# Kernel tuning notes

Hardware: AMD Instinct MI355X
Metric: run time of the kernel (lower is better)

The kernel has to match this reference:

```python
import jax, jax.numpy as jnp
import numpy as np

# config (matches cfg init_kwargs)
FG_THRESH = 0.5
BG_THRESH_LO = 0.1
BG_THRESH_HI = 0.5
N_FG_ROIS = 128
N_ROIS = 512
MEAN = np.array([0.0, 0.0, 0.0, 0.0], dtype=np.float32)
STD = np.array([0.2, 0.2, 0.2, 0.2], dtype=np.float32)

N_PROP = 262144
N_GT = 128


def _make_boxes(key, n, img=1024.0):
    k1, k2 = jax.random.split(key)
    xy = jax.random.uniform(k1, (n, 2), dtype=jnp.float32) * (img - 64.0)
    wh = jax.random.uniform(k2, (n, 2), dtype=jnp.float32) * 192.0 + 8.0
    return jnp.concatenate([xy, xy + wh], axis=-1)  # [n,4] valid x1y1x2y2


def setup_inputs() -> dict:
    key = jax.random.key(0)
    k1, k2, k3 = jax.random.split(key, 3)
    rois = _make_boxes(k1, N_PROP)[None]          # [1, N, 4]
    gt_bbox = _make_boxes(k2, N_GT)[None]         # [1, G, 4]
    labels = jax.random.randint(k3, (1, N_GT), 0, 81, dtype=jnp.int32)  # [1, G]
    return {"rois": rois, "gt_bbox": gt_bbox, "labels": labels}


def _iou_matrix(boxes, gt):
    # boxes [M,4], gt [G,4] -> [M,G] IoU with +1 pixel convention
    bx1, by1, bx2, by2 = boxes[:, 0:1], boxes[:, 1:2], boxes[:, 2:3], boxes[:, 3:4]
    gx1, gy1, gx2, gy2 = gt[None, :, 0], gt[None, :, 1], gt[None, :, 2], gt[None, :, 3]
    iw = jnp.clip(jnp.minimum(bx2, gx2) - jnp.maximum(bx1, gx1) + 1.0, 0.0)
    ih = jnp.clip(jnp.minimum(by2, gy2) - jnp.maximum(by1, gy1) + 1.0, 0.0)
    inter = iw * ih
    area_b = (bx2 - bx1 + 1.0) * (by2 - by1 + 1.0)          # [M,1]
    area_g = (gx2 - gx1 + 1.0) * (gy2 - gy1 + 1.0)          # [1,G]
    return inter / (area_b + area_g - inter)


def _bbox_transform(rois, gt):
    w = rois[:, 2] - rois[:, 0] + 1.0
    h = rois[:, 3] - rois[:, 1] + 1.0
    cx = rois[:, 0] + 0.5 * w
    cy = rois[:, 1] + 0.5 * h
    gw = gt[:, 2] - gt[:, 0] + 1.0
    gh = gt[:, 3] - gt[:, 1] + 1.0
    gcx = gt[:, 0] + 0.5 * gw
    gcy = gt[:, 1] + 0.5 * gh
    return jnp.stack([(gcx - cx) / w, (gcy - cy) / h,
                      jnp.log(gw / w), jnp.log(gh / h)], axis=1)


def _forward(rois, gt_bbox, labels):
    rois = rois[0]          # [N,4]
    gt = gt_bbox[0]         # [G,4]
    lab = labels[0]         # [G]
    all_rois = jnp.concatenate([rois, gt], axis=0)          # [M,4], M=N+G
    ious = _iou_matrix(all_rois, gt)                        # [M,G]  <- dominant traffic
    argmax_row = jnp.argmax(ious, axis=1)                   # [M]
    max_row = jnp.max(ious, axis=1)                         # [M]

    fg = max_row > FG_THRESH
    bg = (max_row > BG_THRESH_LO) & (max_row < BG_THRESH_HI)

    # fixed-size, deterministic variant of the fg/bg sampling:
    # keep first min(N_FG_ROIS, #fg) fg, then fill with bg up to N_ROIS
    fg_cum = jnp.cumsum(fg.astype(jnp.int32))
    sel_fg = fg & (fg_cum <= N_FG_ROIS)
    n_fg = jnp.minimum(N_FG_ROIS, fg_cum[-1])
    bg_cum = jnp.cumsum(bg.astype(jnp.int32))
    sel_bg = bg & (bg_cum <= (N_ROIS - n_fg))

    # stable sort key: fg first (0), then bg (1), then padding rows (2)
    key = jnp.where(sel_fg, 0, jnp.where(sel_bg, 1, 2)).astype(jnp.int32)
    order = jnp.argsort(key, stable=True)
    idx = order[:N_ROIS]                                    # [N_ROIS]

    rois_out = jnp.take(all_rois, idx, axis=0)              # [N_ROIS,4]
    gt_idx = jnp.take(argmax_row, idx)
    labels_out = jnp.take(lab, gt_idx)                      # [N_ROIS]
    gt_out = jnp.take(gt, gt_idx, axis=0)

    delta = _bbox_transform(rois_out, gt_out)
    delta = (delta - jnp.asarray(MEAN)) / jnp.asarray(STD)  # intended normalization
    return rois_out, delta, labels_out


def reference(rois, gt_bbox, labels):
    return _forward(rois, gt_bbox, labels)
```

## Files before the change

### kernel.cpp

```cpp
#include <hip/hip_runtime.h>
#include <stdint.h>

#define N_PROP    262144
#define N_GT      128
#define N_ALL     (N_PROP + N_GT)
#define NFG_MAX   128
#define NROIS_OUT 512
#define BLK       256
#define NBLOCKS   ((N_ALL + BLK - 1) / BLK)

#define OFF_ARGMAX  0
#define OFF_FLAG    524544
#define OFF_BLOCKFG 786816
#define OFF_BLOCKBG 790916
#define OFF_FGOFF   795016
#define OFF_BGOFF   799116
#define OFF_PARAMS  803216

__global__ __launch_bounds__(BLK) void k_iou(
    const float* __restrict__ rois, const float* __restrict__ gt,
    uint16_t* __restrict__ argmax, uint8_t* __restrict__ flag,
    int* __restrict__ blockFg, int* __restrict__ blockBg)
{
    __shared__ float sgx1[N_GT], sgy1[N_GT], sgx2[N_GT], sgy2[N_GT], sga[N_GT];
    int tid = threadIdx.x;
    for (int j = tid; j < N_GT; j += BLK) {
        float4 g = *reinterpret_cast<const float4*>(gt + 4 * j);
        sgx1[j] = g.x; sgy1[j] = g.y; sgx2[j] = g.z; sgy2[j] = g.w;
        sga[j] = __fmul_rn(__fadd_rn(__fsub_rn(g.z, g.x), 1.0f),
                           __fadd_rn(__fsub_rn(g.w, g.y), 1.0f));
    }
    __syncthreads();

    int i = blockIdx.x * BLK + tid;
    bool valid = (i < N_ALL);
    float bx1 = 0.f, by1 = 0.f, bx2 = 0.f, by2 = 0.f;
    if (valid) {
        const float* p = (i < N_PROP) ? (rois + 4 * (size_t)i)
                                      : (gt + 4 * (size_t)(i - N_PROP));
        float4 b = *reinterpret_cast<const float4*>(p);
        bx1 = b.x; by1 = b.y; bx2 = b.z; by2 = b.w;
    }
    float area_b = __fmul_rn(__fadd_rn(__fsub_rn(bx2, bx1), 1.0f),
                             __fadd_rn(__fsub_rn(by2, by1), 1.0f));
    float best = -1.0f; int bestj = 0;
    if (valid) {
        #pragma unroll 4
        for (int j = 0; j < N_GT; ++j) {
            float iw = fmaxf(__fadd_rn(__fsub_rn(fminf(bx2, sgx2[j]), fmaxf(bx1, sgx1[j])), 1.0f), 0.0f);
            float ih = fmaxf(__fadd_rn(__fsub_rn(fminf(by2, sgy2[j]), fmaxf(by1, sgy1[j])), 1.0f), 0.0f);
            float inter = __fmul_rn(iw, ih);
            float denom = __fsub_rn(__fadd_rn(area_b, sga[j]), inter);
            float iou = __fdiv_rn(inter, denom);
            if (iou > best) { best = iou; bestj = j; }
        }
    }
    bool fg = valid && (best > 0.5f);
    bool bg = valid && (best > 0.1f) && (best < 0.5f);
    if (valid) {
        argmax[i] = (uint16_t)bestj;
        flag[i]   = fg ? (uint8_t)0 : (bg ? (uint8_t)1 : (uint8_t)2);
    }
    unsigned long long mf = __ballot(fg ? 1 : 0);
    unsigned long long mb = __ballot(bg ? 1 : 0);
    __shared__ int sF[BLK / 64], sB[BLK / 64];
    int lane = tid & 63, w = tid >> 6;
    if (lane == 0) { sF[w] = __popcll(mf); sB[w] = __popcll(mb); }
    __syncthreads();
    if (tid == 0) {
        int tf = 0, tb = 0;
        for (int k = 0; k < BLK / 64; ++k) { tf += sF[k]; tb += sB[k]; }
        blockFg[blockIdx.x] = tf;
        blockBg[blockIdx.x] = tb;
    }
}

__global__ __launch_bounds__(BLK) void k_scan(
    const int* __restrict__ blockFg, const int* __restrict__ blockBg,
    int* __restrict__ fgOff, int* __restrict__ bgOff, int* __restrict__ params)
{
    __shared__ int sF[BLK], sB[BLK];
    int tid = threadIdx.x;
    int carryF = 0, carryB = 0;
    for (int base = 0; base < NBLOCKS; base += BLK) {
        int idx = base + tid;
        int f = (idx < NBLOCKS) ? blockFg[idx] : 0;
        int b = (idx < NBLOCKS) ? blockBg[idx] : 0;
        sF[tid] = f; sB[tid] = b;
        __syncthreads();
        for (int off = 1; off < BLK; off <<= 1) {
            int vf = (tid >= off) ? sF[tid - off] : 0;
            int vb = (tid >= off) ? sB[tid - off] : 0;
            __syncthreads();
            sF[tid] += vf; sB[tid] += vb;
            __syncthreads();
        }
        if (idx < NBLOCKS) {
            fgOff[idx] = carryF + sF[tid] - f;
            bgOff[idx] = carryB + sB[tid] - b;
        }
        carryF += sF[BLK - 1];
        carryB += sB[BLK - 1];
        __syncthreads();
    }
    if (tid == 0) {
        int fgTot = carryF, bgTot = carryB;
        int NF  = fgTot < NFG_MAX ? fgTot : NFG_MAX;
        int LIM = NROIS_OUT - NF;
        int NB  = bgTot < LIM ? bgTot : LIM;
        params[0] = NF; params[1] = NB; params[2] = LIM;
    }
}

__global__ __launch_bounds__(BLK) void k_select(
    const float* __restrict__ rois, const float* __restrict__ gt,
    const int* __restrict__ labels,
    const uint16_t* __restrict__ argmax, const uint8_t* __restrict__ flag,
    const int* __restrict__ fgOff, const int* __restrict__ bgOff,
    const int* __restrict__ params, float* __restrict__ out)
{
    int tid = threadIdx.x;
    int i = blockIdx.x * BLK + tid;
    bool valid = (i < N_ALL);
    uint8_t f = valid ? flag[i] : (uint8_t)2;
    bool isfg = valid && (f == 0);
    bool isbg = valid && (f == 1);
    unsigned long long mf = __ballot(isfg ? 1 : 0);
    unsigned long long mb = __ballot(isbg ? 1 : 0);
    int lane = tid & 63, w = tid >> 6;
    unsigned long long lemask = (lane == 63) ? ~0ull : ((1ull << (lane + 1)) - 1ull);
    int inclF = __popcll(mf & lemask);
    int inclB = __popcll(mb & lemask);
    __shared__ int sF[BLK / 64], sB[BLK / 64];
    if (lane == 0) { sF[w] = __popcll(mf); sB[w] = __popcll(mb); }
    __syncthreads();
    int preF = 0, preB = 0;
    for (int k = 0; k < w; ++k) { preF += sF[k]; preB += sB[k]; }
    if (!valid) return;

    int fgCum = fgOff[blockIdx.x] + preF + inclF;
    int bgCum = bgOff[blockIdx.x] + preB + inclB;
    int NF = params[0], NB = params[1], LIM = params[2];

    int pos;
    if (isfg && fgCum <= NFG_MAX) {
        pos = fgCum - 1;
    } else if (isbg && bgCum <= LIM) {
        pos = NF + bgCum - 1;
    } else {
        int selF = fgCum < NFG_MAX ? fgCum : NFG_MAX;
        int selB = bgCum < LIM ? bgCum : LIM;
        int restCum = (i + 1) - selF - selB;
        pos = NF + NB + restCum - 1;
    }
    if (pos >= NROIS_OUT) return;

    const float* rp = (i < N_PROP) ? (rois + 4 * (size_t)i)
                                   : (gt + 4 * (size_t)(i - N_PROP));
    float4 r = *reinterpret_cast<const float4*>(rp);
    int g = argmax[i];
    float4 gb = *reinterpret_cast<const float4*>(gt + 4 * (size_t)g);

    float wdt = __fadd_rn(__fsub_rn(r.z, r.x), 1.0f);
    float hgt = __fadd_rn(__fsub_rn(r.w, r.y), 1.0f);
    float cx  = __fadd_rn(r.x, __fmul_rn(0.5f, wdt));
    float cy  = __fadd_rn(r.y, __fmul_rn(0.5f, hgt));
    float gw  = __fadd_rn(__fsub_rn(gb.z, gb.x), 1.0f);
    float gh  = __fadd_rn(__fsub_rn(gb.w, gb.y), 1.0f);
    float gcx = __fadd_rn(gb.x, __fmul_rn(0.5f, gw));
    float gcy = __fadd_rn(gb.y, __fmul_rn(0.5f, gh));

    float d0 = __fdiv_rn(__fsub_rn(gcx, cx), wdt);
    float d1 = __fdiv_rn(__fsub_rn(gcy, cy), hgt);
    float d2 = logf(__fdiv_rn(gw, wdt));
    float d3 = logf(__fdiv_rn(gh, hgt));
    d0 = __fdiv_rn(d0, 0.2f);
    d1 = __fdiv_rn(d1, 0.2f);
    d2 = __fdiv_rn(d2, 0.2f);
    d3 = __fdiv_rn(d3, 0.2f);

    out[4 * pos + 0] = r.x;
    out[4 * pos + 1] = r.y;
    out[4 * pos + 2] = r.z;
    out[4 * pos + 3] = r.w;
    out[2048 + 4 * pos + 0] = d0;
    out[2048 + 4 * pos + 1] = d1;
    out[2048 + 4 * pos + 2] = d2;
    out[2048 + 4 * pos + 3] = d3;
    out[4096 + pos] = (float)labels[g];
}

extern "C" void kernel_launch(void* const* d_in, const int* in_sizes, int n_in,
                              void* d_out, int out_size, void* d_ws, size_t ws_size,
                              hipStream_t stream)
{
    const float* rois   = (const float*)d_in[0];
    const float* gt     = (const float*)d_in[1];
    const int*   labels = (const int*)d_in[2];
    float* out = (float*)d_out;

    char* ws = (char*)d_ws;
    uint16_t* argmax  = (uint16_t*)(ws + OFF_ARGMAX);
    uint8_t*  flag    = (uint8_t*)(ws + OFF_FLAG);
    int*      blockFg = (int*)(ws + OFF_BLOCKFG);
    int*      blockBg = (int*)(ws + OFF_BLOCKBG);
    int*      fgOff   = (int*)(ws + OFF_FGOFF);
    int*      bgOff   = (int*)(ws + OFF_BGOFF);
    int*      params  = (int*)(ws + OFF_PARAMS);

    k_iou<<<NBLOCKS, BLK, 0, stream>>>(rois, gt, argmax, flag, blockFg, blockBg);
    k_scan<<<1, BLK, 0, stream>>>(blockFg, blockBg, fgOff, bgOff, params);
    k_select<<<NBLOCKS, BLK, 0, stream>>>(rois, gt, labels, argmax, flag,
                                          fgOff, bgOff, params, out);
}
```

Measured before the change: 46.56 us.

## Drop scan kernel; compute block prefix offsets redundantly in select kernel

Removes the single-block scan kernel. Each select block now reduces all packed per-block fg/bg counts itself to get its prefix and the totals. It also packs argmax and flag into one 16-bit word, which cuts a global read and write. This saves one launch and a serial single-block stage, at the cost of every one of the ~1025 blocks reading the whole 4 KB count array.

```diff
diff --git a/kernel.cpp b/kernel.cpp
--- a/kernel.cpp
+++ b/kernel.cpp
@@ -9,18 +9,12 @@
 #define BLK       256
 #define NBLOCKS   ((N_ALL + BLK - 1) / BLK)
 
-#define OFF_ARGMAX  0
-#define OFF_FLAG    524544
-#define OFF_BLOCKFG 786816
-#define OFF_BLOCKBG 790916
-#define OFF_FGOFF   795016
-#define OFF_BGOFF   799116
-#define OFF_PARAMS  803216
+#define OFF_PACKED 0
+#define OFF_CNT    524544
 
 __global__ __launch_bounds__(BLK) void k_iou(
     const float* __restrict__ rois, const float* __restrict__ gt,
-    uint16_t* __restrict__ argmax, uint8_t* __restrict__ flag,
-    int* __restrict__ blockFg, int* __restrict__ blockBg)
+    uint16_t* __restrict__ packed, uint32_t* __restrict__ cnt)
 {
     __shared__ float sgx1[N_GT], sgy1[N_GT], sgx2[N_GT], sgy2[N_GT], sga[N_GT];
     int tid = threadIdx.x;
@@ -58,8 +52,8 @@
     bool fg = valid && (best > 0.5f);
     bool bg = valid && (best > 0.1f) && (best < 0.5f);
     if (valid) {
-        argmax[i] = (uint16_t)bestj;
-        flag[i]   = fg ? (uint8_t)0 : (bg ? (uint8_t)1 : (uint8_t)2);
+        int flagv = fg ? 0 : (bg ? 1 : 2);
+        packed[i] = (uint16_t)((flagv << 8) | bestj);
     }
     unsigned long long mf = __ballot(fg ? 1 : 0);
     unsigned long long mb = __ballot(bg ? 1 : 0);
@@ -70,77 +64,68 @@
     if (tid == 0) {
         int tf = 0, tb = 0;
         for (int k = 0; k < BLK / 64; ++k) { tf += sF[k]; tb += sB[k]; }
-        blockFg[blockIdx.x] = tf;
-        blockBg[blockIdx.x] = tb;
-    }
-}
-
-__global__ __launch_bounds__(BLK) void k_scan(
-    const int* __restrict__ blockFg, const int* __restrict__ blockBg,
-    int* __restrict__ fgOff, int* __restrict__ bgOff, int* __restrict__ params)
-{
-    __shared__ int sF[BLK], sB[BLK];
-    int tid = threadIdx.x;
-    int carryF = 0, carryB = 0;
-    for (int base = 0; base < NBLOCKS; base += BLK) {
-        int idx = base + tid;
-        int f = (idx < NBLOCKS) ? blockFg[idx] : 0;
-        int b = (idx < NBLOCKS) ? blockBg[idx] : 0;
-        sF[tid] = f; sB[tid] = b;
-        __syncthreads();
-        for (int off = 1; off < BLK; off <<= 1) {
-            int vf = (tid >= off) ? sF[tid - off] : 0;
-            int vb = (tid >= off) ? sB[tid - off] : 0;
-            __syncthreads();
-            sF[tid] += vf; sB[tid] += vb;
-            __syncthreads();
-        }
-        if (idx < NBLOCKS) {
-            fgOff[idx] = carryF + sF[tid] - f;
-            bgOff[idx] = carryB + sB[tid] - b;
-        }
-        carryF += sF[BLK - 1];
-        carryB += sB[BLK - 1];
-        __syncthreads();
-    }
-    if (tid == 0) {
-        int fgTot = carryF, bgTot = carryB;
-        int NF  = fgTot < NFG_MAX ? fgTot : NFG_MAX;
-        int LIM = NROIS_OUT - NF;
-        int NB  = bgTot < LIM ? bgTot : LIM;
-        params[0] = NF; params[1] = NB; params[2] = LIM;
+        cnt[blockIdx.x] = ((uint32_t)tb << 16) | (uint32_t)tf;
     }
 }
 
 __global__ __launch_bounds__(BLK) void k_select(
     const float* __restrict__ rois, const float* __restrict__ gt,
     const int* __restrict__ labels,
-    const uint16_t* __restrict__ argmax, const uint8_t* __restrict__ flag,
-    const int* __restrict__ fgOff, const int* __restrict__ bgOff,
-    const int* __restrict__ params, float* __restrict__ out)
+    const uint16_t* __restrict__ packed, const uint32_t* __restrict__ cnt,
+    float* __restrict__ out)
 {
-    int tid = threadIdx.x;
-    int i = blockIdx.x * BLK + tid;
+    int tid = threadIdx.x, bid = blockIdx.x;
+    int i = bid * BLK + tid;
     bool valid = (i < N_ALL);
-    uint8_t f = valid ? flag[i] : (uint8_t)2;
-    bool isfg = valid && (f == 0);
-    bool isbg = valid && (f == 1);
+    uint16_t p = valid ? packed[i] : (uint16_t)(2 << 8);
+    int flagv = p >> 8;
+    int g = p & 0xFF;
+    bool isfg = valid && (flagv == 0);
+    bool isbg = valid && (flagv == 1);
+
+    int totF = 0, totB = 0, preF = 0, preB = 0;
+    for (int j = tid; j < NBLOCKS; j += BLK) {
+        uint32_t c = cnt[j];
+        int f = (int)(c & 0xFFFFu), b = (int)(c >> 16);
+        totF += f; totB += b;
+        if (j < bid) { preF += f; preB += b; }
+    }
+    #pragma unroll
+    for (int off = 32; off > 0; off >>= 1) {
+        totF += __shfl_down(totF, off, 64);
+        totB += __shfl_down(totB, off, 64);
+        preF += __shfl_down(preF, off, 64);
+        preB += __shfl_down(preB, off, 64);
+    }
+    __shared__ int sTF[4], sTB[4], sPF[4], sPB[4];
+    __shared__ int sWF[4], sWB[4];
+    int lane = tid & 63, w = tid >> 6;
+    if (lane == 0) { sTF[w] = totF; sTB[w] = totB; sPF[w] = preF; sPB[w] = preB; }
+
     unsigned long long mf = __ballot(isfg ? 1 : 0);
     unsigned long long mb = __ballot(isbg ? 1 : 0);
-    int lane = tid & 63, w = tid >> 6;
     unsigned long long lemask = (lane == 63) ? ~0ull : ((1ull << (lane + 1)) - 1ull);
     int inclF = __popcll(mf & lemask);
     int inclB = __popcll(mb & lemask);
-    __shared__ int sF[BLK / 64], sB[BLK / 64];
-    if (lane == 0) { sF[w] = __popcll(mf); sB[w] = __popcll(mb); }
+    if (lane == 0) { sWF[w] = __popcll(mf); sWB[w] = __popcll(mb); }
     __syncthreads();
-    int preF = 0, preB = 0;
-    for (int k = 0; k < w; ++k) { preF += sF[k]; preB += sB[k]; }
+
+    totF = sTF[0] + sTF[1] + sTF[2] + sTF[3];
+    totB = sTB[0] + sTB[1] + sTB[2] + sTB[3];
+    preF = sPF[0] + sPF[1] + sPF[2] + sPF[3];
+    preB = sPB[0] + sPB[1] + sPB[2] + sPB[3];
+    int wPreF = 0, wPreB = 0;
+    for (int k = 0; k < 4; ++k) {
+        if (k < w) { wPreF += sWF[k]; wPreB += sWB[k]; }
+    }
     if (!valid) return;
 
-    int fgCum = fgOff[blockIdx.x] + preF + inclF;
-    int bgCum = bgOff[blockIdx.x] + preB + inclB;
-    int NF = params[0], NB = params[1], LIM = params[2];
+    int NF  = totF < NFG_MAX ? totF : NFG_MAX;
+    int LIM = NROIS_OUT - NF;
+    int NB  = totB < LIM ? totB : LIM;
+
+    int fgCum = preF + wPreF + inclF;
+    int bgCum = preB + wPreB + inclB;
 
     int pos;
     if (isfg && fgCum <= NFG_MAX) {
@@ -158,7 +143,6 @@
     const float* rp = (i < N_PROP) ? (rois + 4 * (size_t)i)
                                    : (gt + 4 * (size_t)(i - N_PROP));
     float4 r = *reinterpret_cast<const float4*>(rp);
-    int g = argmax[i];
     float4 gb = *reinterpret_cast<const float4*>(gt + 4 * (size_t)g);
 
     float wdt = __fadd_rn(__fsub_rn(r.z, r.x), 1.0f);
@@ -170,14 +154,10 @@
     float gcx = __fadd_rn(gb.x, __fmul_rn(0.5f, gw));
     float gcy = __fadd_rn(gb.y, __fmul_rn(0.5f, gh));
 
-    float d0 = __fdiv_rn(__fsub_rn(gcx, cx), wdt);
-    float d1 = __fdiv_rn(__fsub_rn(gcy, cy), hgt);
-    float d2 = logf(__fdiv_rn(gw, wdt));
-    float d3 = logf(__fdiv_rn(gh, hgt));
-    d0 = __fdiv_rn(d0, 0.2f);
-    d1 = __fdiv_rn(d1, 0.2f);
-    d2 = __fdiv_rn(d2, 0.2f);
-    d3 = __fdiv_rn(d3, 0.2f);
+    float d0 = __fdiv_rn(__fdiv_rn(__fsub_rn(gcx, cx), wdt), 0.2f);
+    float d1 = __fdiv_rn(__fdiv_rn(__fsub_rn(gcy, cy), hgt), 0.2f);
+    float d2 = __fdiv_rn(logf(__fdiv_rn(gw, wdt)), 0.2f);
+    float d3 = __fdiv_rn(logf(__fdiv_rn(gh, hgt)), 0.2f);
 
     out[4 * pos + 0] = r.x;
     out[4 * pos + 1] = r.y;
@@ -200,16 +180,9 @@
     float* out = (float*)d_out;
 
     char* ws = (char*)d_ws;
-    uint16_t* argmax  = (uint16_t*)(ws + OFF_ARGMAX);
-    uint8_t*  flag    = (uint8_t*)(ws + OFF_FLAG);
-    int*      blockFg = (int*)(ws + OFF_BLOCKFG);
-    int*      blockBg = (int*)(ws + OFF_BLOCKBG);
-    int*      fgOff   = (int*)(ws + OFF_FGOFF);
-    int*      bgOff   = (int*)(ws + OFF_BGOFF);
-    int*      params  = (int*)(ws + OFF_PARAMS);
+    uint16_t* packed = (uint16_t*)(ws + OFF_PACKED);
+    uint32_t* cnt    = (uint32_t*)(ws + OFF_CNT);
 
-    k_iou<<<NBLOCKS, BLK, 0, stream>>>(rois, gt, argmax, flag, blockFg, blockBg);
-    k_scan<<<1, BLK, 0, stream>>>(blockFg, blockBg, fgOff, bgOff, params);
-    k_select<<<NBLOCKS, BLK, 0, stream>>>(rois, gt, labels, argmax, flag,
-                                          fgOff, bgOff, params, out);
+    k_iou<<<NBLOCKS, BLK, 0, stream>>>(rois, gt, packed, cnt);
+    k_select<<<NBLOCKS, BLK, 0, stream>>>(rois, gt, labels, packed, cnt, out);
 }
```

Result: faster. 40.58 us (-12.9%).
